# Kernel optimization log

Measured on AMD Instinct MI355X. Metric: run time of the kernel, lower is better.

Reference implementation:

```python
import jax, jax.numpy as jnp
import numpy as np


def _mlp(x, Ws):
    # torch Linear(bias=False): y = x @ W.T, then leaky_relu (slope 0.01)
    for W in Ws:
        x = jax.nn.leaky_relu(x @ W.T)
    return x


def setup_inputs() -> dict:
    key = jax.random.key(0)
    ks = jax.random.split(key, 17)
    B, Cm, Hm = 128, 512, 28
    D = 2048  # NET_OUT_DIM['resnet50']
    shapes = {
        'x_mid': (B, Cm, Hm, Hm),
        'x_deep': (B, D, 7, 7),
        'w_shallow': (D, Cm),
        'ow1': (1024, D), 'ow2': (512, 1024), 'ow3': (64, 512),
        'sw1': (1024, D), 'sw2': (512, 1024), 'sw3': (64, 512),
        'tw1': (64, 128), 'tw2': (64, 64),
        'cw1': (64, 128), 'cw2': (64, 64),
        'qw1': (64, 64), 'qw2': (64, 64),
        'center': (64,), 'proto': (4, 64),
    }
    out = {}
    for k, (name, shp) in zip(ks, shapes.items()):
        scale = 1.0 if name in ('x_mid', 'x_deep', 'center', 'proto') else 0.02
        out[name] = jax.random.normal(k, shp, dtype=jnp.float32) * scale
    return out


def reference(x_mid, x_deep, w_shallow, ow1, ow2, ow3, sw1, sw2, sw3,
              tw1, tw2, cw1, cw2, qw1, qw2, center, proto):
    # shallow_conv: 1x1 conv Cm -> D
    shallow_map = jnp.einsum('bchw,oc->bohw', x_mid, w_shallow)
    # adaptive avgpool (1,1) + flatten == mean over HW
    origin = _mlp(x_deep.mean(axis=(2, 3)), [ow1, ow2, ow3])        # [B,64]
    shallow = _mlp(shallow_map.mean(axis=(2, 3)), [sw1, sw2, sw3])  # [B,64]
    texture = _mlp(jnp.concatenate([shallow, shallow - center[None]], axis=1),
                   [tw1, tw2])                                      # [B,64]
    # squared distances to each domain prototype -> [B, domain_cnt]
    sim = jnp.sum((texture[:, None, :] - proto[None, :, :]) ** 2, axis=-1)
    category = jnp.argmax(sim, axis=1)  # argmax(softmax(x)) == argmax(x)
    logp = jax.nn.log_softmax(sim, axis=1)
    ce = -jnp.mean(jnp.take_along_axis(logp, category[:, None], axis=1))
    # vectorized gather of per-sample prototype (replaces python loop)
    class_feat = jnp.concatenate([origin, origin - proto[category]], axis=1)
    class_feat = _mlp(class_feat, [cw1, cw2])
    class_svdd = jnp.sum((class_feat - center[None]) ** 2, axis=1)
    origin_svdd = jnp.sum((_mlp(origin, [qw1, qw2]) - center[None]) ** 2, axis=1)
    align = jnp.abs(origin_svdd - class_svdd)
    return jnp.stack([ce, origin_svdd.mean(), class_svdd.mean(),
                      align.mean()]).reshape(4, 1)
```

## Files before the change

kernel.cpp:

```cpp
#include <hip/hip_runtime.h>
#include <hip/hip_bf16.h>
#include <math.h>

typedef __attribute__((ext_vector_type(8))) short bf16x8;
typedef __attribute__((ext_vector_type(4))) float f32x4;

__device__ __forceinline__ float leaky(float x) { return x > 0.0f ? x : 0.01f * x; }

__device__ __forceinline__ unsigned short f2b(float f) {
    unsigned u = __builtin_bit_cast(unsigned, f);
    u += 0x7fffu + ((u >> 16) & 1u);
    return (unsigned short)(u >> 16);
}

__device__ __forceinline__ bf16x8 cvt8(float4 u0, float4 u1) {
    bf16x8 r;
    r[0] = (short)f2b(u0.x); r[1] = (short)f2b(u0.y);
    r[2] = (short)f2b(u0.z); r[3] = (short)f2b(u0.w);
    r[4] = (short)f2b(u1.x); r[5] = (short)f2b(u1.y);
    r[6] = (short)f2b(u1.z); r[7] = (short)f2b(u1.w);
    return r;
}

__global__ __launch_bounds__(256) void means_kernel(const float* __restrict__ xm,
                                                    const float* __restrict__ xd,
                                                    unsigned short* __restrict__ xm_b,
                                                    unsigned short* __restrict__ xd_b,
                                                    float4* __restrict__ zbase)
{
    int blk = blockIdx.x;
    int tid = threadIdx.x;
    if (blk >= 32768) {
        int idx = (blk - 32768) * 256 + tid;
        zbase[idx] = make_float4(0.f, 0.f, 0.f, 0.f);
        return;
    }
    if (blk < 16384) {
        int lane = tid & 63;
        int wid  = tid >> 6;
        int row  = blk * 4 + wid;
        const float4* r = (const float4*)(xm + (size_t)row * 784);
        float s = 0.0f;
        for (int i = lane; i < 196; i += 64) {
            float4 v = r[i];
            s += v.x + v.y + v.z + v.w;
        }
        #pragma unroll
        for (int off = 32; off; off >>= 1) s += __shfl_xor(s, off);
        if (lane == 0) xm_b[row] = f2b(s * (1.0f / 784.0f));
    } else {
        int b2  = blk - 16384;
        int sub = tid & 15;
        int r   = tid >> 4;
        int row = b2 * 16 + r;
        const float* base = xd + (size_t)row * 49;
        float s = base[sub] + base[sub + 16] + base[sub + 32];
        if (sub == 0) s += base[48];
        #pragma unroll
        for (int off = 8; off; off >>= 1) s += __shfl_xor(s, off);
        if (sub == 0) xd_b[row] = f2b(s * (1.0f / 49.0f));
    }
}

__global__ __launch_bounds__(512) void gemm_ldsb(
    const void* __restrict__ A0, int a0f, int a0act,
    const void* __restrict__ A1, int a1f, int a1act,
    const float* __restrict__ B0, const float* __restrict__ B1,
    float* __restrict__ C0, float* __restrict__ C1c,
    int N, int K, int S)
{
    __shared__ unsigned short Bs[32][72];

    const int z = blockIdx.z;
    const void*  A    = z ? A1 : A0;
    const int    af   = z ? a1f : a0f;
    const int    aact = z ? a1act : a0act;
    const float* B    = z ? B1 : B0;
    float*       C    = z ? C1c : C0;

    const int n0 = blockIdx.x * 32;
    const int Kc = K / S;
    const int k0 = blockIdx.y * Kc;

    const int tid = threadIdx.x;
    const int l  = tid & 63;
    const int lr = l & 15;
    const int lc = l >> 4;
    const int m0 = (tid >> 6) * 16;
    const int srow = tid >> 4;
    const int scol = (tid & 15) * 4;

    f32x4 acc0 = {0.f,0.f,0.f,0.f}, acc1 = {0.f,0.f,0.f,0.f};

    for (int kt = 0; kt < Kc; kt += 64) {
        float4 v = *(const float4*)(B + (size_t)(n0 + srow) * K + k0 + kt + scol);
        __syncthreads();
        Bs[srow][scol + 0] = f2b(v.x);
        Bs[srow][scol + 1] = f2b(v.y);
        Bs[srow][scol + 2] = f2b(v.z);
        Bs[srow][scol + 3] = f2b(v.w);
        __syncthreads();

        #pragma unroll
        for (int kc = 0; kc < 2; ++kc) {
            size_t aoff = (size_t)(m0 + lr) * K + k0 + kt + kc * 32 + lc * 8;
            bf16x8 a;
            if (!af) {
                a = *(const bf16x8*)((const unsigned short*)A + aoff);
            } else {
                const float* p = (const float*)A + aoff;
                float4 u0 = *(const float4*)p;
                float4 u1 = *(const float4*)(p + 4);
                if (aact) {
                    u0.x = leaky(u0.x); u0.y = leaky(u0.y);
                    u0.z = leaky(u0.z); u0.w = leaky(u0.w);
                    u1.x = leaky(u1.x); u1.y = leaky(u1.y);
                    u1.z = leaky(u1.z); u1.w = leaky(u1.w);
                }
                a = cvt8(u0, u1);
            }
            bf16x8 b0 = *(const bf16x8*)&Bs[lr][kc * 32 + lc * 8];
            bf16x8 b1 = *(const bf16x8*)&Bs[16 + lr][kc * 32 + lc * 8];
            acc0 = __builtin_amdgcn_mfma_f32_16x16x32_bf16(a, b0, acc0, 0, 0, 0);
            acc1 = __builtin_amdgcn_mfma_f32_16x16x32_bf16(a, b1, acc1, 0, 0, 0);
        }
    }

    #pragma unroll
    for (int r = 0; r < 4; ++r) {
        int m = m0 + lc * 4 + r;
        atomicAdd(&C[(size_t)m * N + n0 + lr],      acc0[r]);
        atomicAdd(&C[(size_t)m * N + n0 + 16 + lr], acc1[r]);
    }
}

__global__ __launch_bounds__(256) void tail_kernel(
    const float* __restrict__ C3o, const float* __restrict__ C3s,
    const float* __restrict__ ow3, const float* __restrict__ sw3,
    const float* __restrict__ tw1, const float* __restrict__ tw2,
    const float* __restrict__ cw1, const float* __restrict__ cw2,
    const float* __restrict__ qw1, const float* __restrict__ qw2,
    const float* __restrict__ center, const float* __restrict__ proto,
    float* __restrict__ ce_t, float* __restrict__ osv,
    float* __restrict__ csv, float* __restrict__ alv)
{
    const int b = blockIdx.x;
    const int t = threadIdx.x;
    __shared__ float o2r[512], s2r[512];
    __shared__ float red[2][64][4];
    __shared__ float o3s[64], s3s[64], t1s[64], c1s[64], q1s[64];

    for (int e = t; e < 512; e += 256) {
        o2r[e] = leaky(C3o[b * 512 + e]);
        s2r[e] = leaky(C3s[b * 512 + e]);
    }
    __syncthreads();

    {
        int o = t & 63, q = t >> 6;
        const float* wro = ow3 + (size_t)o * 512 + q * 128;
        const float* wrs = sw3 + (size_t)o * 512 + q * 128;
        const float* xo = o2r + q * 128;
        const float* xs = s2r + q * 128;
        float ao = 0.f, as_ = 0.f;
        for (int j = 0; j < 128; ++j) {
            ao  += wro[j] * xo[j];
            as_ += wrs[j] * xs[j];
        }
        red[0][o][q] = ao;
        red[1][o][q] = as_;
    }
    __syncthreads();
    if (t < 64) {
        o3s[t] = leaky(red[0][t][0] + red[0][t][1] + red[0][t][2] + red[0][t][3]);
        s3s[t] = leaky(red[1][t][0] + red[1][t][1] + red[1][t][2] + red[1][t][3]);
    }
    __syncthreads();

    float ce_val = 0.f;
    int o = t;
    if (t < 64) {
        float acc = 0.f;
        for (int j = 0; j < 64; ++j) acc += tw1[o * 128 + j] * s3s[j];
        for (int j = 0; j < 64; ++j) acc += tw1[o * 128 + 64 + j] * (s3s[j] - center[j]);
        t1s[o] = leaky(acc);
    }
    __syncthreads();
    if (t < 64) {
        float acc = 0.f;
        for (int j = 0; j < 64; ++j) acc += tw2[o * 64 + j] * t1s[j];
        float tex = leaky(acc);
        float sim[4];
        #pragma unroll
        for (int k = 0; k < 4; ++k) {
            float d = tex - proto[k * 64 + o];
            float v = d * d;
            #pragma unroll
            for (int off = 32; off; off >>= 1) v += __shfl_xor(v, off);
            sim[k] = v;
        }
        int cat = 0; float best = sim[0];
        #pragma unroll
        for (int k = 1; k < 4; ++k) if (sim[k] > best) { best = sim[k]; cat = k; }
        float sume = 0.f;
        #pragma unroll
        for (int k = 0; k < 4; ++k) sume += expf(sim[k] - best);
        ce_val = logf(sume);
        acc = 0.f;
        for (int j = 0; j < 64; ++j) acc += cw1[o * 128 + j] * o3s[j];
        for (int j = 0; j < 64; ++j) acc += cw1[o * 128 + 64 + j] * (o3s[j] - proto[cat * 64 + j]);
        c1s[o] = leaky(acc);
        acc = 0.f;
        for (int j = 0; j < 64; ++j) acc += qw1[o * 64 + j] * o3s[j];
        q1s[o] = leaky(acc);
    }
    __syncthreads();
    if (t < 64) {
        float acc = 0.f;
        for (int j = 0; j < 64; ++j) acc += cw2[o * 64 + j] * c1s[j];
        float cf = leaky(acc);
        float dc = cf - center[o];
        float cs = dc * dc;
        #pragma unroll
        for (int off = 32; off; off >>= 1) cs += __shfl_xor(cs, off);
        acc = 0.f;
        for (int j = 0; j < 64; ++j) acc += qw2[o * 64 + j] * q1s[j];
        float qf = leaky(acc);
        float dq = qf - center[o];
        float os = dq * dq;
        #pragma unroll
        for (int off = 32; off; off >>= 1) os += __shfl_xor(os, off);
        if (o == 0) {
            ce_t[b] = ce_val;
            osv[b]  = os;
            csv[b]  = cs;
            alv[b]  = fabsf(os - cs);
        }
    }
}

__global__ __launch_bounds__(128) void finalize_kernel(
    const float* __restrict__ ce_t, const float* __restrict__ osv,
    const float* __restrict__ csv, const float* __restrict__ alv,
    float* __restrict__ out)
{
    int t = threadIdx.x;
    float v[4] = { ce_t[t], osv[t], csv[t], alv[t] };
    __shared__ float tmp[4][2];
    int lane = t & 63, w = t >> 6;
    #pragma unroll
    for (int i = 0; i < 4; ++i) {
        float x = v[i];
        #pragma unroll
        for (int off = 32; off; off >>= 1) x += __shfl_xor(x, off);
        if (lane == 0) tmp[i][w] = x;
    }
    __syncthreads();
    if (t < 4) out[t] = (tmp[t][0] + tmp[t][1]) * (1.0f / 128.0f);
}

extern "C" void kernel_launch(void* const* d_in, const int* in_sizes, int n_in,
                              void* d_out, int out_size, void* d_ws, size_t ws_size,
                              hipStream_t stream)
{
    const float* x_mid     = (const float*)d_in[0];
    const float* x_deep    = (const float*)d_in[1];
    const float* w_shallow = (const float*)d_in[2];
    const float* ow1 = (const float*)d_in[3];
    const float* ow2 = (const float*)d_in[4];
    const float* ow3 = (const float*)d_in[5];
    const float* sw1 = (const float*)d_in[6];
    const float* sw2 = (const float*)d_in[7];
    const float* sw3 = (const float*)d_in[8];
    const float* tw1 = (const float*)d_in[9];
    const float* tw2 = (const float*)d_in[10];
    const float* cw1 = (const float*)d_in[11];
    const float* cw2 = (const float*)d_in[12];
    const float* qw1 = (const float*)d_in[13];
    const float* qw2 = (const float*)d_in[14];
    const float* center = (const float*)d_in[15];
    const float* proto  = (const float*)d_in[16];
    float* out = (float*)d_out;

    float* wf = (float*)d_ws;
    float* C1  = wf;
    float* C2o = wf + 262144;
    float* C2s = wf + 393216;
    float* C3o = wf + 524288;
    float* C3s = wf + 589824;
    unsigned short* xm_b = (unsigned short*)(wf + 655360);
    unsigned short* xd_b = (unsigned short*)((char*)xm_b + 131072);
    float* ce_t = (float*)((char*)xm_b + 131072 + 524288);
    float* osv  = ce_t + 128;
    float* csv  = ce_t + 256;
    float* alv  = ce_t + 384;

    means_kernel<<<33408, 256, 0, stream>>>(x_mid, x_deep, xm_b, xd_b, (float4*)wf);

    gemm_ldsb<<<dim3(64, 4, 1), 512, 0, stream>>>(
        xm_b, 0, 0, xm_b, 0, 0, w_shallow, w_shallow, C1, C1, 2048, 512, 4);

    gemm_ldsb<<<dim3(32, 8, 2), 512, 0, stream>>>(
        xd_b, 0, 0, C1, 1, 0, ow1, sw1, C2o, C2s, 1024, 2048, 8);

    gemm_ldsb<<<dim3(16, 8, 2), 512, 0, stream>>>(
        C2o, 1, 1, C2s, 1, 1, ow2, sw2, C3o, C3s, 512, 1024, 8);

    tail_kernel<<<128, 256, 0, stream>>>(C3o, C3s, ow3, sw3, tw1, tw2, cw1, cw2,
                                         qw1, qw2, center, proto, ce_t, osv, csv, alv);

    finalize_kernel<<<1, 128, 0, stream>>>(ce_t, osv, csv, alv, out);
}
```

Baseline: 97.86 us.

## Fuse GEMM chain, tail and finalize into one kernel with atomic-counter gating

Replaces the three GEMM launches, the tail kernel and the finalize kernel with one fused kernel. Block ranges run different phases, and each phase waits on global atomic counters before it starts. The independent origin-path GEMM can run alongside the shallow conv GEMM, and a last-block-done pattern performs the final reduction. This removes launch gaps and inter-kernel barriers, at the cost of spin-waiting blocks and reliance on in-order block dispatch and counter reset in the means kernel.

```diff
diff --git a/kernel.cpp b/kernel.cpp
--- a/kernel.cpp
+++ b/kernel.cpp
@@ -62,27 +62,20 @@
     }
 }
 
-__global__ __launch_bounds__(512) void gemm_ldsb(
-    const void* __restrict__ A0, int a0f, int a0act,
-    const void* __restrict__ A1, int a1f, int a1act,
-    const float* __restrict__ B0, const float* __restrict__ B1,
-    float* __restrict__ C0, float* __restrict__ C1c,
-    int N, int K, int S)
+__device__ __forceinline__ void gate(int* cnt, int target) {
+    if (threadIdx.x == 0) {
+        while (__hip_atomic_load(cnt, __ATOMIC_ACQUIRE, __HIP_MEMORY_SCOPE_AGENT) < target)
+            __builtin_amdgcn_s_sleep(8);
+    }
+    __syncthreads();
+}
+
+__device__ __forceinline__ void gemm_phase(
+    const void* __restrict__ A, int af, int aact,
+    const float* __restrict__ B, float* __restrict__ C,
+    int N, int K, int Kc, int k0, int n0,
+    unsigned short (*Bs)[72], int tid)
 {
-    __shared__ unsigned short Bs[32][72];
-
-    const int z = blockIdx.z;
-    const void*  A    = z ? A1 : A0;
-    const int    af   = z ? a1f : a0f;
-    const int    aact = z ? a1act : a0act;
-    const float* B    = z ? B1 : B0;
-    float*       C    = z ? C1c : C0;
-
-    const int n0 = blockIdx.x * 32;
-    const int Kc = K / S;
-    const int k0 = blockIdx.y * Kc;
-
-    const int tid = threadIdx.x;
     const int l  = tid & 63;
     const int lr = l & 15;
     const int lc = l >> 4;
@@ -134,59 +127,105 @@
     }
 }
 
-__global__ __launch_bounds__(256) void tail_kernel(
-    const float* __restrict__ C3o, const float* __restrict__ C3s,
-    const float* __restrict__ ow3, const float* __restrict__ sw3,
+__global__ __launch_bounds__(512, 4) void fused_kernel(
+    float* __restrict__ wf,
+    const unsigned short* __restrict__ xm_b, const unsigned short* __restrict__ xd_b,
+    const float* __restrict__ w_shallow,
+    const float* __restrict__ ow1, const float* __restrict__ ow2, const float* __restrict__ ow3,
+    const float* __restrict__ sw1, const float* __restrict__ sw2, const float* __restrict__ sw3,
     const float* __restrict__ tw1, const float* __restrict__ tw2,
     const float* __restrict__ cw1, const float* __restrict__ cw2,
     const float* __restrict__ qw1, const float* __restrict__ qw2,
     const float* __restrict__ center, const float* __restrict__ proto,
-    float* __restrict__ ce_t, float* __restrict__ osv,
-    float* __restrict__ csv, float* __restrict__ alv)
+    float* __restrict__ out)
 {
-    const int b = blockIdx.x;
-    const int t = threadIdx.x;
+    __shared__ unsigned short Bs[32][72];
     __shared__ float o2r[512], s2r[512];
     __shared__ float red[2][64][4];
     __shared__ float o3s[64], s3s[64], t1s[64], c1s[64], q1s[64];
-
-    for (int e = t; e < 512; e += 256) {
+    __shared__ float tmp[4][8];
+    __shared__ int flag;
+
+    float* C1  = wf;
+    float* C2o = wf + 262144;
+    float* C2s = wf + 393216;
+    float* C3o = wf + 524288;
+    float* C3s = wf + 589824;
+    int*   cnt = (int*)(wf + 655360);
+    float* ce_t = wf + 655616;
+    float* osv  = ce_t + 128;
+    float* csv  = ce_t + 256;
+    float* alv  = ce_t + 384;
+
+    const int bid = blockIdx.x;
+    const int tid = threadIdx.x;
+
+    if (bid < 256) {
+        int nt = bid >> 2, s = bid & 3;
+        gemm_phase(xm_b, 0, 0, w_shallow, C1, 2048, 512, 128, s * 128, nt * 32, Bs, tid);
+        __syncthreads();
+        if (tid == 0) __hip_atomic_fetch_add(&cnt[0], 1, __ATOMIC_RELEASE, __HIP_MEMORY_SCOPE_AGENT);
+        return;
+    }
+    if (bid < 768) {
+        int b2 = bid - 256;
+        int z = b2 >> 8, idx = b2 & 255, nt = idx >> 3, s = idx & 7;
+        if (z == 0) {
+            gemm_phase(xd_b, 0, 0, ow1, C2o, 1024, 2048, 256, s * 256, nt * 32, Bs, tid);
+        } else {
+            gate(&cnt[0], 256);
+            gemm_phase(C1, 1, 0, sw1, C2s, 1024, 2048, 256, s * 256, nt * 32, Bs, tid);
+        }
+        __syncthreads();
+        if (tid == 0) __hip_atomic_fetch_add(&cnt[1], 1, __ATOMIC_RELEASE, __HIP_MEMORY_SCOPE_AGENT);
+        return;
+    }
+    if (bid < 1024) {
+        int b3 = bid - 768;
+        int z = b3 >> 7, idx = b3 & 127, nt = idx >> 3, s = idx & 7;
+        gate(&cnt[1], 512);
+        gemm_phase(z ? C2s : C2o, 1, 1, z ? sw2 : ow2, z ? C3s : C3o,
+                   512, 1024, 128, s * 128, nt * 32, Bs, tid);
+        __syncthreads();
+        if (tid == 0) __hip_atomic_fetch_add(&cnt[2], 1, __ATOMIC_RELEASE, __HIP_MEMORY_SCOPE_AGENT);
+        return;
+    }
+
+    const int b = bid - 1024;
+    gate(&cnt[2], 256);
+
+    {
+        int e = tid;
         o2r[e] = leaky(C3o[b * 512 + e]);
         s2r[e] = leaky(C3s[b * 512 + e]);
     }
     __syncthreads();
-
     {
-        int o = t & 63, q = t >> 6;
-        const float* wro = ow3 + (size_t)o * 512 + q * 128;
-        const float* wrs = sw3 + (size_t)o * 512 + q * 128;
-        const float* xo = o2r + q * 128;
-        const float* xs = s2r + q * 128;
-        float ao = 0.f, as_ = 0.f;
-        for (int j = 0; j < 128; ++j) {
-            ao  += wro[j] * xo[j];
-            as_ += wrs[j] * xs[j];
-        }
-        red[0][o][q] = ao;
-        red[1][o][q] = as_;
-    }
-    __syncthreads();
-    if (t < 64) {
-        o3s[t] = leaky(red[0][t][0] + red[0][t][1] + red[0][t][2] + red[0][t][3]);
-        s3s[t] = leaky(red[1][t][0] + red[1][t][1] + red[1][t][2] + red[1][t][3]);
+        int p = tid >> 8, o = (tid >> 2) & 63, q = tid & 3;
+        const float* wr = (p ? sw3 : ow3) + (size_t)o * 512 + q * 128;
+        const float* xr = (p ? s2r : o2r) + q * 128;
+        float acc = 0.f;
+        for (int j = 0; j < 128; ++j) acc += wr[j] * xr[j];
+        red[p][o][q] = acc;
+    }
+    __syncthreads();
+    if (tid < 128) {
+        int p = tid >> 6, o = tid & 63;
+        float v = leaky(red[p][o][0] + red[p][o][1] + red[p][o][2] + red[p][o][3]);
+        if (p) s3s[o] = v; else o3s[o] = v;
     }
     __syncthreads();
 
     float ce_val = 0.f;
-    int o = t;
-    if (t < 64) {
+    int o = tid;
+    if (tid < 64) {
         float acc = 0.f;
         for (int j = 0; j < 64; ++j) acc += tw1[o * 128 + j] * s3s[j];
         for (int j = 0; j < 64; ++j) acc += tw1[o * 128 + 64 + j] * (s3s[j] - center[j]);
         t1s[o] = leaky(acc);
     }
     __syncthreads();
-    if (t < 64) {
+    if (tid < 64) {
         float acc = 0.f;
         for (int j = 0; j < 64; ++j) acc += tw2[o * 64 + j] * t1s[j];
         float tex = leaky(acc);
@@ -206,16 +245,16 @@
         #pragma unroll
         for (int k = 0; k < 4; ++k) sume += expf(sim[k] - best);
         ce_val = logf(sume);
-        acc = 0.f;
-        for (int j = 0; j < 64; ++j) acc += cw1[o * 128 + j] * o3s[j];
-        for (int j = 0; j < 64; ++j) acc += cw1[o * 128 + 64 + j] * (o3s[j] - proto[cat * 64 + j]);
-        c1s[o] = leaky(acc);
-        acc = 0.f;
-        for (int j = 0; j < 64; ++j) acc += qw1[o * 64 + j] * o3s[j];
-        q1s[o] = leaky(acc);
-    }
-    __syncthreads();
-    if (t < 64) {
+        float acc2 = 0.f;
+        for (int j = 0; j < 64; ++j) acc2 += cw1[o * 128 + j] * o3s[j];
+        for (int j = 0; j < 64; ++j) acc2 += cw1[o * 128 + 64 + j] * (o3s[j] - proto[cat * 64 + j]);
+        c1s[o] = leaky(acc2);
+        acc2 = 0.f;
+        for (int j = 0; j < 64; ++j) acc2 += qw1[o * 64 + j] * o3s[j];
+        q1s[o] = leaky(acc2);
+    }
+    __syncthreads();
+    if (tid < 64) {
         float acc = 0.f;
         for (int j = 0; j < 64; ++j) acc += cw2[o * 64 + j] * c1s[j];
         float cf = leaky(acc);
@@ -231,32 +270,43 @@
         #pragma unroll
         for (int off = 32; off; off >>= 1) os += __shfl_xor(os, off);
         if (o == 0) {
-            ce_t[b] = ce_val;
-            osv[b]  = os;
-            csv[b]  = cs;
-            alv[b]  = fabsf(os - cs);
-        }
-    }
-}
-
-__global__ __launch_bounds__(128) void finalize_kernel(
-    const float* __restrict__ ce_t, const float* __restrict__ osv,
-    const float* __restrict__ csv, const float* __restrict__ alv,
-    float* __restrict__ out)
-{
-    int t = threadIdx.x;
-    float v[4] = { ce_t[t], osv[t], csv[t], alv[t] };
-    __shared__ float tmp[4][2];
-    int lane = t & 63, w = t >> 6;
-    #pragma unroll
-    for (int i = 0; i < 4; ++i) {
-        float x = v[i];
-        #pragma unroll
-        for (int off = 32; off; off >>= 1) x += __shfl_xor(x, off);
-        if (lane == 0) tmp[i][w] = x;
-    }
-    __syncthreads();
-    if (t < 4) out[t] = (tmp[t][0] + tmp[t][1]) * (1.0f / 128.0f);
+            __hip_atomic_store(&ce_t[b], ce_val, __ATOMIC_RELAXED, __HIP_MEMORY_SCOPE_AGENT);
+            __hip_atomic_store(&osv[b],  os,     __ATOMIC_RELAXED, __HIP_MEMORY_SCOPE_AGENT);
+            __hip_atomic_store(&csv[b],  cs,     __ATOMIC_RELAXED, __HIP_MEMORY_SCOPE_AGENT);
+            __hip_atomic_store(&alv[b],  fabsf(os - cs), __ATOMIC_RELAXED, __HIP_MEMORY_SCOPE_AGENT);
+        }
+    }
+    __syncthreads();
+    if (tid == 0) {
+        int old = __hip_atomic_fetch_add(&cnt[3], 1, __ATOMIC_ACQ_REL, __HIP_MEMORY_SCOPE_AGENT);
+        flag = (old == 127);
+    }
+    __syncthreads();
+    if (flag) {
+        float v0 = 0.f, v1 = 0.f, v2 = 0.f, v3 = 0.f;
+        if (tid < 128) {
+            v0 = __hip_atomic_load(&ce_t[tid], __ATOMIC_RELAXED, __HIP_MEMORY_SCOPE_AGENT);
+            v1 = __hip_atomic_load(&osv[tid],  __ATOMIC_RELAXED, __HIP_MEMORY_SCOPE_AGENT);
+            v2 = __hip_atomic_load(&csv[tid],  __ATOMIC_RELAXED, __HIP_MEMORY_SCOPE_AGENT);
+            v3 = __hip_atomic_load(&alv[tid],  __ATOMIC_RELAXED, __HIP_MEMORY_SCOPE_AGENT);
+        }
+        float v[4] = { v0, v1, v2, v3 };
+        int lane = tid & 63, wv = tid >> 6;
+        #pragma unroll
+        for (int i = 0; i < 4; ++i) {
+            float x = v[i];
+            #pragma unroll
+            for (int off = 32; off; off >>= 1) x += __shfl_xor(x, off);
+            if (lane == 0) tmp[i][wv] = x;
+        }
+        __syncthreads();
+        if (tid < 4) {
+            float s = 0.f;
+            #pragma unroll
+            for (int j = 0; j < 8; ++j) s += tmp[tid][j];
+            out[tid] = s * (1.0f / 128.0f);
+        }
+    }
 }
 
 extern "C" void kernel_launch(void* const* d_in, const int* in_sizes, int n_in,
@@ -283,31 +333,13 @@
     float* out = (float*)d_out;
 
     float* wf = (float*)d_ws;
-    float* C1  = wf;
-    float* C2o = wf + 262144;
-    float* C2s = wf + 393216;
-    float* C3o = wf + 524288;
-    float* C3s = wf + 589824;
-    unsigned short* xm_b = (unsigned short*)(wf + 655360);
+    unsigned short* xm_b = (unsigned short*)(wf + 656384);
     unsigned short* xd_b = (unsigned short*)((char*)xm_b + 131072);
-    float* ce_t = (float*)((char*)xm_b + 131072 + 524288);
-    float* osv  = ce_t + 128;
-    float* csv  = ce_t + 256;
-    float* alv  = ce_t + 384;
-
-    means_kernel<<<33408, 256, 0, stream>>>(x_mid, x_deep, xm_b, xd_b, (float4*)wf);
-
-    gemm_ldsb<<<dim3(64, 4, 1), 512, 0, stream>>>(
-        xm_b, 0, 0, xm_b, 0, 0, w_shallow, w_shallow, C1, C1, 2048, 512, 4);
-
-    gemm_ldsb<<<dim3(32, 8, 2), 512, 0, stream>>>(
-        xd_b, 0, 0, C1, 1, 0, ow1, sw1, C2o, C2s, 1024, 2048, 8);
-
-    gemm_ldsb<<<dim3(16, 8, 2), 512, 0, stream>>>(
-        C2o, 1, 1, C2s, 1, 1, ow2, sw2, C3o, C3s, 512, 1024, 8);
-
-    tail_kernel<<<128, 256, 0, stream>>>(C3o, C3s, ow3, sw3, tw1, tw2, cw1, cw2,
-                                         qw1, qw2, center, proto, ce_t, osv, csv, alv);
-
-    finalize_kernel<<<1, 128, 0, stream>>>(ce_t, osv, csv, alv, out);
-}
+
+    means_kernel<<<33409, 256, 0, stream>>>(x_mid, x_deep, xm_b, xd_b, (float4*)wf);
+
+    fused_kernel<<<1152, 512, 0, stream>>>(wf, xm_b, xd_b, w_shallow,
+                                           ow1, ow2, ow3, sw1, sw2, sw3,
+                                           tw1, tw2, cw1, cw2, qw1, qw2,
+                                           center, proto, out);
+}
```

Result: slower. 183.6 us (+87.7%).
